# Kernel tuning notes

Hardware: AMD Instinct MI355X
Metric: run time of the kernel (lower is better)

## Reference

```python
import jax, jax.numpy as jnp
import numpy as np

IMG_W, IMG_H = 704, 256
BN_EPS, LN_EPS = 1e-5, 1e-5


def _l2norm(x, axis):
    n = jnp.linalg.norm(x, axis=axis, keepdims=True)
    return x / jnp.maximum(n, 1e-12)


def _layernorm(x, g, b):
    m = jnp.mean(x, axis=-1, keepdims=True)
    v = jnp.var(x, axis=-1, keepdims=True)
    return (x - m) / jnp.sqrt(v + LN_EPS) * g + b


def _bilinear(ref, uv):
    # ref: (B, d, H, W); uv: (B, P, 2) pixel coords (x, y)
    B, d, H, W = ref.shape
    x, y = uv[..., 0], uv[..., 1]
    x0 = jnp.floor(x); y0 = jnp.floor(y)
    wx = x - x0; wy = y - y0
    valid = (x >= 0) & (x <= W - 1) & (y >= 0) & (y <= H - 1)
    x0i = jnp.clip(x0.astype(jnp.int32), 0, W - 1)
    x1i = jnp.clip(x0i + 1, 0, W - 1)
    y0i = jnp.clip(y0.astype(jnp.int32), 0, H - 1)
    y1i = jnp.clip(y0i + 1, 0, H - 1)
    ref_t = ref.reshape(B, d, H * W).transpose(0, 2, 1)  # (B, HW, d)
    g = lambda yy, xx: jnp.take_along_axis(ref_t, (yy * W + xx)[..., None], axis=1)
    val = (g(y0i, x0i) * ((1 - wx) * (1 - wy))[..., None]
           + g(y0i, x1i) * (wx * (1 - wy))[..., None]
           + g(y1i, x0i) * ((1 - wx) * wy)[..., None]
           + g(y1i, x1i) * (wx * wy)[..., None])  # (B, P, d)
    return val, valid.astype(ref.dtype)


def setup_inputs() -> dict:
    key = jax.random.key(0)
    ks = jax.random.split(key, 12)
    b, n, fd, dim, h, w = 2, 6, 128, 128, 64, 176
    feature = jax.random.normal(ks[0], (b, n, fd, h, w), jnp.float32)
    # intrinsics ~ [[500,0,352],[0,500,128],[0,0,1]]
    K = jnp.array([[500.0, 0.0, IMG_W / 2], [0.0, 500.0, IMG_H / 2], [0.0, 0.0, 1.0]], jnp.float32)
    I_src = jnp.broadcast_to(K, (b, n, 3, 3)).copy()
    I_tar_inv = jnp.broadcast_to(jnp.linalg.inv(K), (b, 3, 3)).copy()
    # extrinsics near identity: small rotation + small translation
    a = 0.02 * jax.random.normal(ks[1], (b, n, 3), jnp.float32)
    zeros = jnp.zeros((b, n), jnp.float32)
    skew = jnp.stack([
        jnp.stack([zeros, -a[..., 2], a[..., 1]], -1),
        jnp.stack([a[..., 2], zeros, -a[..., 0]], -1),
        jnp.stack([-a[..., 1], a[..., 0], zeros], -1)], -2)
    R = jnp.eye(3, dtype=jnp.float32) + skew
    T = 0.1 * jax.random.normal(ks[2], (b, n, 3, 1), jnp.float32)
    E = jnp.broadcast_to(jnp.eye(4, dtype=jnp.float32), (b, n, 4, 4)).copy()
    E = E.at[..., :3, :3].set(R).at[..., :3, 3:4].set(T)
    dis = 1.5 * jnp.ones((b, 1, 1, 1), jnp.float32)
    norm = jnp.array([0.0, 0.0, 1.0], jnp.float32)[None, None] + 0.01 * jax.random.normal(ks[3], (b, 1, 3), jnp.float32)
    s = 1.0 / np.sqrt(fd)
    return {
        'feature': feature, 'I_src': I_src, 'I_tar_inv': I_tar_inv, 'E': E, 'dis': dis, 'norm': norm,
        'conv_w': s * jax.random.normal(ks[4], (dim, fd), jnp.float32),
        'bn_gamma': jnp.ones((fd,), jnp.float32), 'bn_beta': jnp.zeros((fd,), jnp.float32),
        'bn_mean': 0.1 * jax.random.normal(ks[5], (fd,), jnp.float32),
        'bn_var': jax.random.uniform(ks[6], (fd,), jnp.float32, 0.5, 1.5),
        'ln1_g': jnp.ones((dim,), jnp.float32), 'ln1_b': jnp.zeros((dim,), jnp.float32),
        'ln2_g': jnp.ones((dim,), jnp.float32), 'ln2_b': jnp.zeros((dim,), jnp.float32),
        'mlp_w1': s * jax.random.normal(ks[7], (dim, 2 * dim), jnp.float32),
        'mlp_b1': jnp.zeros((2 * dim,), jnp.float32),
        'mlp_w2': (1.0 / np.sqrt(2 * fd)) * jax.random.normal(ks[8], (2 * dim, dim), jnp.float32),
        'mlp_b2': jnp.zeros((dim,), jnp.float32),
    }


def reference(feature, I_src, I_tar_inv, E, dis, norm, conv_w, bn_gamma, bn_beta, bn_mean, bn_var,
              ln1_g, ln1_b, ln2_g, ln2_b, mlp_w1, mlp_b1, mlp_w2, mlp_b2):
    b, n, fd, h, w = feature.shape
    dim = conv_w.shape[0]
    P = h * w
    # ---- pixel grid in [0,1], homogeneous ----
    xs = jnp.linspace(0.0, 1.0, w, dtype=feature.dtype)
    ys = jnp.linspace(0.0, 1.0, h, dtype=feature.dtype)
    X, Y = jnp.meshgrid(xs, ys)  # (h, w), x varies along width
    pix = jnp.stack([X, Y, jnp.ones_like(X)], 0).reshape(3, P)  # (3, P)
    img_wh1 = jnp.array([[IMG_W], [IMG_H], [1.0]], feature.dtype)  # (3,1)
    pix = pix * img_wh1
    # ---- homography H = I_src (R - T n^T / dis) I_tar_inv ----
    R = E[..., :3, :3]
    T = E[..., :3, 3:4]
    Hm = I_src @ (R - (T @ norm[:, None, :, :]) / dis) @ I_tar_inv[:, None, :, :]  # (b,n,3,3)
    homo = jnp.einsum('bnij,jp->bnip', Hm, pix)  # (b,n,3,P)
    homo = homo[:, :, :2] / homo[:, :, 2:]
    homo = homo / img_wh1[:2]  # back to 0..1
    uv = homo.transpose(0, 1, 3, 2).reshape(b * n, P, 2) * jnp.array([w, h], feature.dtype)
    # ---- feature_linear: BN(eval) -> ReLU -> 1x1 conv ----
    xf = (feature - bn_mean[:, None, None]) / jnp.sqrt(bn_var + BN_EPS)[:, None, None]
    xf = xf * bn_gamma[:, None, None] + bn_beta[:, None, None]
    xf = jax.nn.relu(xf)
    val = jnp.einsum('oc,bnchw->bnohw', conv_w, xf)  # (b,n,dim,h,w)
    query = val[:, 0]  # (b,dim,h,w)
    # ---- homography-guided bilinear sampling ----
    v, mask = _bilinear(val.reshape(b * n, dim, h, w), uv)  # (bn,P,dim), (bn,P)
    key_n = _l2norm(v, axis=2).reshape(b, n, P, dim)
    q = _l2norm(query.reshape(b, dim, P), axis=1)
    dot = jnp.einsum('bdp,bnpd->bnp', q, key_n)
    dot = dot * mask.reshape(b, n, P)
    att = jax.nn.softmax(dot, axis=1)
    z = jnp.einsum('bnp,bnpd->bpd', att, v.reshape(b, n, P, dim))
    z = z.transpose(0, 2, 1).reshape(b, dim, h, w)
    z = query + z
    # ---- MLP block ----
    z = z.reshape(b, dim, P).transpose(0, 2, 1)  # (b,P,dim)
    z = _layernorm(z, ln1_g, ln1_b)
    hdn = jax.nn.gelu(z @ mlp_w1 + mlp_b1, approximate=False)
    z = z + (hdn @ mlp_w2 + mlp_b2)
    z = _layernorm(z, ln2_g, ln2_b)
    return z.transpose(0, 2, 1).reshape(b, dim, h, w)
```

## Files before the change

### kernel.cpp

```cpp
#include <hip/hip_runtime.h>
#include <hip/hip_bf16.h>
#include <cstdint>
#include <cstddef>

#define B_   2
#define N_   6
#define FD_  128
#define DIM_ 128
#define H_   64
#define W_   176
#define P_   (H_*W_)
#define IMGW 704.0
#define IMGH 256.0
#define UVB  8

struct __align__(16) Samp { float wx, wy; int o00, o01; int o10, o11; int valid, pad; };

typedef __attribute__((ext_vector_type(8))) short short8;
typedef __attribute__((ext_vector_type(4))) float f32x4;

__device__ __forceinline__ float wave_sum(float v) {
#pragma unroll
  for (int off = 32; off > 0; off >>= 1) v += __shfl_xor(v, off, 64);
  return v;
}

__device__ __forceinline__ unsigned short f2bf(float f) {
  union { __hip_bfloat16 h; unsigned short u; } c;
  c.h = __float2bfloat16(f);
  return c.u;
}
__device__ __forceinline__ float bf2f(unsigned short s) {
  return __uint_as_float(((unsigned int)s) << 16);
}
__device__ __forceinline__ float bfx(uint2 u, int j) {
  unsigned int w = (j < 2) ? u.x : u.y;
  return bf2f((unsigned short)((j & 1) ? (w >> 16) : (w & 0xffffu)));
}

__global__ __launch_bounds__(256) void prep_kernel(const float* __restrict__ I_src, const float* __restrict__ I_tar_inv,
                           const float* __restrict__ E, const float* __restrict__ dis,
                           const float* __restrict__ nrm,
                           const float* __restrict__ bn_g, const float* __restrict__ bn_b,
                           const float* __restrict__ bn_m, const float* __restrict__ bn_v,
                           const float* __restrict__ w1, const float* __restrict__ w2,
                           const float* __restrict__ conv_w,
                           Samp* __restrict__ samp, float* __restrict__ bns, float* __restrict__ bnb,
                           short* __restrict__ w1b, short* __restrict__ w2b, short* __restrict__ cwb) {
  int blk = blockIdx.x;
  if (blk >= B_ * N_ * UVB) {
    int tid = (blk - B_ * N_ * UVB) * 256 + threadIdx.x;
    int f = tid >> 6, l = tid & 63;
    if (f < 64) {
      int nt = f >> 2, ks = f & 3;
      int n = nt * 16 + (l & 15);
      int kb = ks * 32 + (l >> 4) * 8;
#pragma unroll
      for (int j = 0; j < 8; ++j)
        w1b[((size_t)f * 64 + l) * 8 + j] = (short)f2bf(w1[(size_t)(kb + j) * 256 + n]);
    } else if (f < 128) {
      int g = f - 64;
      int nt = g >> 3, ks = g & 7;
      int n = nt * 16 + (l & 15);
      int kb = ks * 32 + (l >> 4) * 8;
#pragma unroll
      for (int j = 0; j < 8; ++j)
        w2b[((size_t)g * 64 + l) * 8 + j] = (short)f2bf(w2[(size_t)(kb + j) * 128 + n]);
    } else {
      int g2 = f - 128;
      int ot = g2 >> 2, ks = g2 & 3;
      int o  = ot * 16 + (l & 15);
      int cb = ks * 32 + (l >> 4) * 8;
#pragma unroll
      for (int j = 0; j < 8; ++j)
        cwb[((size_t)g2 * 64 + l) * 8 + j] = (short)f2bf(conv_w[(size_t)o * FD_ + cb + j]);
    }
    return;
  }
  int bn = blk / UVB;
  int part = blk % UVB;
  int bb = bn / N_;
  if (blk == 0 && threadIdx.x < FD_) {
    int t = threadIdx.x;
    float inv = 1.0f / sqrtf(bn_v[t] + 1e-5f);
    float sc = bn_g[t] * inv;
    bns[t] = sc;
    bnb[t] = bn_b[t] - bn_m[t] * sc;
  }
  const float* Ep = E + bn * 16;
  double R[9], T[3];
#pragma unroll
  for (int i = 0; i < 3; ++i) {
#pragma unroll
    for (int j = 0; j < 3; ++j) R[i*3+j] = (double)Ep[i*4+j];
    T[i] = (double)Ep[i*4+3];
  }
  double dd = (double)dis[bb];
  double M[9];
#pragma unroll
  for (int i = 0; i < 3; ++i)
#pragma unroll
    for (int j = 0; j < 3; ++j)
      M[i*3+j] = R[i*3+j] - T[i] * (double)nrm[bb*3+j] / dd;
  const float* Is = I_src + bn * 9;
  double A[9];
#pragma unroll
  for (int i = 0; i < 3; ++i)
#pragma unroll
    for (int j = 0; j < 3; ++j)
      A[i*3+j] = (double)Is[i*3+0]*M[0+j] + (double)Is[i*3+1]*M[3+j] + (double)Is[i*3+2]*M[6+j];
  const float* It = I_tar_inv + bb * 9;
  double Hm[9];
#pragma unroll
  for (int i = 0; i < 3; ++i)
#pragma unroll
    for (int j = 0; j < 3; ++j)
      Hm[i*3+j] = A[i*3+0]*(double)It[0+j] + A[i*3+1]*(double)It[3+j] + A[i*3+2]*(double)It[6+j];

  const double dx = 1.0 / (double)(W_ - 1);
  const double dy = 1.0 / (double)(H_ - 1);
  for (int p = part * 256 + threadIdx.x; p < P_; p += 256 * UVB) {
    int ii = p / W_;
    int jj = p - ii * W_;
    double xs = (jj == W_ - 1) ? 1.0 : (double)jj * dx;
    double ys = (ii == H_ - 1) ? 1.0 : (double)ii * dy;
    double px = xs * IMGW;
    double py = ys * IMGH;
    double hx = Hm[0]*px + Hm[1]*py + Hm[2];
    double hy = Hm[3]*px + Hm[4]*py + Hm[5];
    double hz = Hm[6]*px + Hm[7]*py + Hm[8];
    double u = ((hx / hz) / IMGW) * (double)W_;
    double v = ((hy / hz) / IMGH) * (double)H_;
    double x0 = floor(u), y0 = floor(v);
    bool valid = (u >= 0.0) && (u <= (double)(W_ - 1)) && (v >= 0.0) && (v <= (double)(H_ - 1));
    int x0i = min(max((int)x0, 0), W_ - 1);
    int x1i = min(x0i + 1, W_ - 1);
    int y0i = min(max((int)y0, 0), H_ - 1);
    int y1i = min(y0i + 1, H_ - 1);
    Samp s;
    s.wx = (float)(u - x0);
    s.wy = (float)(v - y0);
    s.o00 = (y0i * W_ + x0i) * DIM_;
    s.o01 = (y0i * W_ + x1i) * DIM_;
    s.o10 = (y1i * W_ + x0i) * DIM_;
    s.o11 = (y1i * W_ + x1i) * DIM_;
    s.valid = valid ? 1 : 0;
    s.pad = 0;
    samp[(size_t)bn * P_ + p] = s;
  }
}

__global__ __launch_bounds__(256) void conv_kernel(const float* __restrict__ feature,
    const short* __restrict__ cwb, const float* __restrict__ bns_g, const float* __restrict__ bnb_g,
    unsigned short* __restrict__ val_t) {
  __shared__ float bns_s[FD_], bnb_s[FD_];
  int t = threadIdx.x;
  if (t < FD_) { bns_s[t] = bns_g[t]; bnb_s[t] = bnb_g[t]; }
  __syncthreads();

  int bn = blockIdx.y;
  int p0 = blockIdx.x * 64;
  int lane = t & 63, wv = t >> 6;
  int m = lane & 15, quad = lane >> 4;
  int pw = wv * 16;

  const float* fb = feature + (size_t)bn * FD_ * P_ + p0 + pw + m;

  float xv[4][8];
#pragma unroll
  for (int ks = 0; ks < 4; ++ks)
#pragma unroll
    for (int j = 0; j < 8; ++j) {
      int c = ks * 32 + quad * 8 + j;
      xv[ks][j] = fb[(size_t)c * P_];
    }

  short8 Ah[4], Al[4];
#pragma unroll
  for (int ks = 0; ks < 4; ++ks)
#pragma unroll
    for (int j = 0; j < 8; ++j) {
      int c = ks * 32 + quad * 8 + j;
      float v = fmaxf(xv[ks][j] * bns_s[c] + bnb_s[c], 0.f);
      unsigned short h = f2bf(v);
      Ah[ks][j] = (short)h;
      Al[ks][j] = (short)f2bf(v - bf2f(h));
    }

  f32x4 acc[8];
#pragma unroll
  for (int ot = 0; ot < 8; ++ot) {
    f32x4 a = {0.f, 0.f, 0.f, 0.f};
#pragma unroll
    for (int ks = 0; ks < 4; ++ks) {
      short8 Bv = *(const short8*)(cwb + ((size_t)(ot * 4 + ks) * 64 + lane) * 8);
      a = __builtin_amdgcn_mfma_f32_16x16x32_bf16(Ah[ks], Bv, a, 0, 0, 0);
      a = __builtin_amdgcn_mfma_f32_16x16x32_bf16(Al[ks], Bv, a, 0, 0, 0);
    }
    acc[ot] = a;
  }

  unsigned short* vb = val_t + ((size_t)bn * P_ + p0 + pw + quad * 4) * DIM_ + m;
#pragma unroll
  for (int ot = 0; ot < 8; ++ot)
#pragma unroll
    for (int r = 0; r < 4; ++r)
      vb[(size_t)r * DIM_ + ot * 16] = f2bf(acc[ot][r]);
}

__global__ __launch_bounds__(256) void attn_kernel(const unsigned short* __restrict__ val_t,
    const Samp* __restrict__ samp,
    const float* __restrict__ ln1g, const float* __restrict__ ln1b,
    float* __restrict__ zln) {
  int lane = threadIdx.x & 63;
  int wv = threadIdx.x >> 6;
  int half = lane >> 5;
  int sl = lane & 31;
  int bid = blockIdx.x;
  int newbid = (bid & 7) * (gridDim.x >> 3) + (bid >> 3);
  int pt = newbid * 8 + wv * 2 + half;
  int bb = pt / P_;
  int p = pt - bb * P_;
  int d0 = sl << 2;

  uint2 uq = *(const uint2*)(val_t + ((size_t)(bb * N_) * P_ + p) * DIM_ + d0);
  float qv[4] = { bfx(uq, 0), bfx(uq, 1), bfx(uq, 2), bfx(uq, 3) };
  float qss = qv[0]*qv[0] + qv[1]*qv[1] + qv[2]*qv[2] + qv[3]*qv[3];
#pragma unroll
  for (int off = 1; off <= 16; off <<= 1) qss += __shfl_xor(qss, off, 64);
  float qinv = 1.0f / fmaxf(sqrtf(qss), 1e-12f);

  float dots[N_], vs[N_][4];
#pragma unroll
  for (int n = 0; n < N_; ++n) {
    Samp s = samp[(size_t)(bb * N_ + n) * P_ + p];
    const unsigned short* base = val_t + (size_t)(bb * N_ + n) * P_ * DIM_ + d0;
    uint2 u00 = *(const uint2*)(base + s.o00);
    uint2 u01 = *(const uint2*)(base + s.o01);
    uint2 u10 = *(const uint2*)(base + s.o10);
    uint2 u11 = *(const uint2*)(base + s.o11);
    float wx = s.wx, wy = s.wy;
    float w00 = (1.0f - wx) * (1.0f - wy), w01 = wx * (1.0f - wy);
    float w10 = (1.0f - wx) * wy,          w11 = wx * wy;
    float ss = 0.f, du = 0.f;
#pragma unroll
    for (int j = 0; j < 4; ++j) {
      float v = bfx(u00, j) * w00 + bfx(u01, j) * w01 + bfx(u10, j) * w10 + bfx(u11, j) * w11;
      vs[n][j] = v;
      ss += v * v;
      du += qv[j] * v;
    }
#pragma unroll
    for (int off = 1; off <= 16; off <<= 1) {
      ss += __shfl_xor(ss, off, 64);
      du += __shfl_xor(du, off, 64);
    }
    float kinv = 1.0f / fmaxf(sqrtf(ss), 1e-12f);
    dots[n] = s.valid ? (du * kinv * qinv) : 0.0f;
  }
  float mx = dots[0];
#pragma unroll
  for (int n = 1; n < N_; ++n) mx = fmaxf(mx, dots[n]);
  float es[N_], den = 0.f;
#pragma unroll
  for (int n = 0; n < N_; ++n) { es[n] = expf(dots[n] - mx); den += es[n]; }
  float dinv = 1.0f / den;
  float z[4] = { qv[0], qv[1], qv[2], qv[3] };
#pragma unroll
  for (int n = 0; n < N_; ++n) {
    float a = es[n] * dinv;
#pragma unroll
    for (int j = 0; j < 4; ++j) z[j] += a * vs[n][j];
  }
  float sz = z[0] + z[1] + z[2] + z[3];
  float q2 = z[0]*z[0] + z[1]*z[1] + z[2]*z[2] + z[3]*z[3];
#pragma unroll
  for (int off = 1; off <= 16; off <<= 1) {
    sz += __shfl_xor(sz, off, 64);
    q2 += __shfl_xor(q2, off, 64);
  }
  float mean = sz * (1.0f / DIM_);
  float var = fmaxf(q2 * (1.0f / DIM_) - mean * mean, 0.f);
  float rstd = rsqrtf(var + 1e-5f);
  float4 g4 = *(const float4*)(ln1g + d0);
  float4 b4 = *(const float4*)(ln1b + d0);
  float4 o4;
  o4.x = (z[0] - mean) * rstd * g4.x + b4.x;
  o4.y = (z[1] - mean) * rstd * g4.y + b4.y;
  o4.z = (z[2] - mean) * rstd * g4.z + b4.z;
  o4.w = (z[3] - mean) * rstd * g4.w + b4.w;
  *(float4*)(zln + (size_t)pt * DIM_ + d0) = o4;
}

__global__ __launch_bounds__(64) void mlp_kernel(const float* __restrict__ zln,
    const short* __restrict__ w1b, const short* __restrict__ w2b,
    const float* __restrict__ b1, const float* __restrict__ b2,
    const float* __restrict__ ln2g, const float* __restrict__ ln2b,
    float* __restrict__ out) {
  __shared__ __align__(16) char smem[16896];
  short* hh = (short*)smem;
  short* hl = (short*)(smem + 8448);
  float* zo = (float*)smem;

  int l = threadIdx.x;
  int m = l & 15, quad = l >> 4;
  int row0 = blockIdx.x * 16;

  const float* zr0 = zln + (size_t)(row0 + m) * DIM_;
  short8 A1h[4], A1l[4];
#pragma unroll
  for (int ks = 0; ks < 4; ++ks) {
    float4 xa = *(const float4*)(zr0 + ks * 32 + quad * 8);
    float4 xb = *(const float4*)(zr0 + ks * 32 + quad * 8 + 4);
    float v[8] = {xa.x, xa.y, xa.z, xa.w, xb.x, xb.y, xb.z, xb.w};
#pragma unroll
    for (int j = 0; j < 8; ++j) {
      unsigned short h = f2bf(v[j]);
      A1h[ks][j] = (short)h;
      A1l[ks][j] = (short)f2bf(v[j] - bf2f(h));
    }
  }

  float res[8][4];
#pragma unroll
  for (int dt = 0; dt < 8; ++dt)
#pragma unroll
    for (int r = 0; r < 4; ++r)
      res[dt][r] = zln[(size_t)(row0 + quad * 4 + r) * DIM_ + dt * 16 + m];

  float b1v[16];
#pragma unroll
  for (int nt = 0; nt < 16; ++nt) b1v[nt] = b1[nt * 16 + m];
  float b2v[8], g2v[8], be2v[8];
#pragma unroll
  for (int dt = 0; dt < 8; ++dt) {
    int d = dt * 16 + m;
    b2v[dt] = b2[d]; g2v[dt] = ln2g[d]; be2v[dt] = ln2b[d];
  }

#pragma unroll
  for (int nt = 0; nt < 16; ++nt) {
    f32x4 a = {0.f, 0.f, 0.f, 0.f};
#pragma unroll
    for (int ks = 0; ks < 4; ++ks) {
      short8 Bv = *(const short8*)(w1b + ((size_t)(nt * 4 + ks) * 64 + l) * 8);
      a = __builtin_amdgcn_mfma_f32_16x16x32_bf16(A1h[ks], Bv, a, 0, 0, 0);
      a = __builtin_amdgcn_mfma_f32_16x16x32_bf16(A1l[ks], Bv, a, 0, 0, 0);
    }
#pragma unroll
    for (int r = 0; r < 4; ++r) {
      float hv = a[r] + b1v[nt];
      float g = 0.5f * hv * (1.0f + erff(hv * 0.70710678118654752f));
      unsigned short gh = f2bf(g);
      int addr = (quad * 4 + r) * 264 + nt * 16 + m;
      hh[addr] = (short)gh;
      hl[addr] = (short)f2bf(g - bf2f(gh));
    }
  }
  __syncthreads();

  f32x4 acc2[8];
#pragma unroll
  for (int dt = 0; dt < 8; ++dt) acc2[dt] = (f32x4){0.f, 0.f, 0.f, 0.f};
#pragma unroll
  for (int ks2 = 0; ks2 < 8; ++ks2) {
    short8 A2h = *(const short8*)&hh[m * 264 + ks2 * 32 + quad * 8];
    short8 A2l = *(const short8*)&hl[m * 264 + ks2 * 32 + quad * 8];
#pragma unroll
    for (int dt = 0; dt < 8; ++dt) {
      short8 Bv = *(const short8*)(w2b + ((size_t)(dt * 8 + ks2) * 64 + l) * 8);
      acc2[dt] = __builtin_amdgcn_mfma_f32_16x16x32_bf16(A2h, Bv, acc2[dt], 0, 0, 0);
      acc2[dt] = __builtin_amdgcn_mfma_f32_16x16x32_bf16(A2l, Bv, acc2[dt], 0, 0, 0);
    }
  }

  float z2[8][4];
#pragma unroll
  for (int dt = 0; dt < 8; ++dt)
#pragma unroll
    for (int r = 0; r < 4; ++r)
      z2[dt][r] = acc2[dt][r] + b2v[dt] + res[dt][r];

  float mean[4], rstd[4];
#pragma unroll
  for (int r = 0; r < 4; ++r) {
    float s = 0.f, q2 = 0.f;
#pragma unroll
    for (int dt = 0; dt < 8; ++dt) { float z = z2[dt][r]; s += z; q2 += z * z; }
#pragma unroll
    for (int off = 1; off <= 8; off <<= 1) {
      s  += __shfl_xor(s,  off, 64);
      q2 += __shfl_xor(q2, off, 64);
    }
    mean[r] = s * (1.0f / 128.0f);
    float var = fmaxf(q2 * (1.0f / 128.0f) - mean[r] * mean[r], 0.f);
    rstd[r] = rsqrtf(var + 1e-5f);
  }
  __syncthreads();

#pragma unroll
  for (int dt = 0; dt < 8; ++dt)
#pragma unroll
    for (int r = 0; r < 4; ++r) {
      float v = (z2[dt][r] - mean[r]) * rstd[r] * g2v[dt] + be2v[dt];
      zo[(dt * 16 + m) * 20 + quad * 4 + r] = v;
    }
  __syncthreads();

  int bb2 = row0 / P_;
  int p0 = row0 - bb2 * P_;
  float* ob = out + (size_t)bb2 * DIM_ * P_ + p0;
#pragma unroll
  for (int pass = 0; pass < 8; ++pass) {
    int idx = pass * 64 + l;
    int d = idx >> 2, fq = idx & 3;
    float4 v4 = *(float4*)&zo[d * 20 + fq * 4];
    *(float4*)(ob + (size_t)d * P_ + fq * 4) = v4;
  }
}

extern "C" void kernel_launch(void* const* d_in, const int* in_sizes, int n_in,
                              void* d_out, int out_size, void* d_ws, size_t ws_size,
                              hipStream_t stream) {
  const float* feature = (const float*)d_in[0];
  const float* I_src   = (const float*)d_in[1];
  const float* I_tar   = (const float*)d_in[2];
  const float* E       = (const float*)d_in[3];
  const float* dis     = (const float*)d_in[4];
  const float* nrm     = (const float*)d_in[5];
  const float* conv_w  = (const float*)d_in[6];
  const float* bn_g    = (const float*)d_in[7];
  const float* bn_b    = (const float*)d_in[8];
  const float* bn_m    = (const float*)d_in[9];
  const float* bn_v    = (const float*)d_in[10];
  const float* ln1g    = (const float*)d_in[11];
  const float* ln1b    = (const float*)d_in[12];
  const float* ln2g    = (const float*)d_in[13];
  const float* ln2b    = (const float*)d_in[14];
  const float* w1      = (const float*)d_in[15];
  const float* b1      = (const float*)d_in[16];
  const float* w2      = (const float*)d_in[17];
  const float* b2      = (const float*)d_in[18];
  float* out = (float*)d_out;

  float* wsf = (float*)d_ws;
  float* bns = wsf;
  float* bnb = wsf + 128;
  unsigned short* val_t = (unsigned short*)(wsf + 256);
  float* zln = (float*)(val_t + (size_t)B_ * N_ * P_ * DIM_);
  Samp*  samp = (Samp*)(zln + (size_t)B_ * P_ * DIM_);
  short* w1b = (short*)(samp + (size_t)B_ * N_ * P_);
  short* w2b = w1b + 32768;
  short* cwb = w2b + 32768;

  hipLaunchKernelGGL(prep_kernel, dim3(B_ * N_ * UVB + 40), dim3(256), 0, stream,
                     I_src, I_tar, E, dis, nrm, bn_g, bn_b, bn_m, bn_v, w1, w2, conv_w,
                     samp, bns, bnb, w1b, w2b, cwb);
  hipLaunchKernelGGL(conv_kernel, dim3(P_ / 64, B_ * N_), dim3(256), 0, stream,
                     feature, cwb, bns, bnb, val_t);
  hipLaunchKernelGGL(attn_kernel, dim3(B_ * P_ / 8), dim3(256), 0, stream,
                     val_t, samp, ln1g, ln1b, zln);
  hipLaunchKernelGGL(mlp_kernel, dim3(B_ * P_ / 16), dim3(64), 0, stream,
                     zln, w1b, w2b, b1, b2, ln2g, ln2b, out);
}
```

Before: 211.2 us.

## Split MLP kernel work across four waves per 16-row block

The MLP kernel now launches 256 threads per block instead of 64. Each of the four waves computes a quarter of the hidden-layer N-tiles and a quarter of the output D-tiles, and the LayerNorm row statistics are reduced across waves through a small shared-memory buffer. The goal is to cut per-wave register pressure and serial MFMA chain length and to raise parallelism per block. The cost is an extra barrier, and every wave redundantly loads the A fragments and splits them into hi/lo parts.

```diff
diff --git a/kernel.cpp b/kernel.cpp
--- a/kernel.cpp
+++ b/kernel.cpp
@@ -292,17 +292,19 @@
   *(float4*)(zln + (size_t)pt * DIM_ + d0) = o4;
 }
 
-__global__ __launch_bounds__(64) void mlp_kernel(const float* __restrict__ zln,
+__global__ __launch_bounds__(256) void mlp_kernel(const float* __restrict__ zln,
     const short* __restrict__ w1b, const short* __restrict__ w2b,
     const float* __restrict__ b1, const float* __restrict__ b2,
     const float* __restrict__ ln2g, const float* __restrict__ ln2b,
     float* __restrict__ out) {
-  __shared__ __align__(16) char smem[16896];
+  __shared__ __align__(16) char smem[17408];
   short* hh = (short*)smem;
   short* hl = (short*)(smem + 8448);
+  float* pbuf = (float*)(smem + 16896);
   float* zo = (float*)smem;
 
-  int l = threadIdx.x;
+  int t = threadIdx.x;
+  int l = t & 63, ng = t >> 6;
   int m = l & 15, quad = l >> 4;
   int row0 = blockIdx.x * 16;
 
@@ -321,25 +323,23 @@
     }
   }
 
-  float res[8][4];
-#pragma unroll
-  for (int dt = 0; dt < 8; ++dt)
+  float b1v[4];
+#pragma unroll
+  for (int i = 0; i < 4; ++i) b1v[i] = b1[(ng * 4 + i) * 16 + m];
+  float res[2][4], b2v[2], g2v[2], be2v[2];
+#pragma unroll
+  for (int e = 0; e < 2; ++e) {
+    int dt = ng * 2 + e;
+    int d = dt * 16 + m;
+    b2v[e] = b2[d]; g2v[e] = ln2g[d]; be2v[e] = ln2b[d];
 #pragma unroll
     for (int r = 0; r < 4; ++r)
-      res[dt][r] = zln[(size_t)(row0 + quad * 4 + r) * DIM_ + dt * 16 + m];
-
-  float b1v[16];
-#pragma unroll
-  for (int nt = 0; nt < 16; ++nt) b1v[nt] = b1[nt * 16 + m];
-  float b2v[8], g2v[8], be2v[8];
-#pragma unroll
-  for (int dt = 0; dt < 8; ++dt) {
-    int d = dt * 16 + m;
-    b2v[dt] = b2[d]; g2v[dt] = ln2g[d]; be2v[dt] = ln2b[d];
-  }
-
-#pragma unroll
-  for (int nt = 0; nt < 16; ++nt) {
+      res[e][r] = zln[(size_t)(row0 + quad * 4 + r) * DIM_ + dt * 16 + m];
+  }
+
+#pragma unroll
+  for (int i = 0; i < 4; ++i) {
+    int nt = ng * 4 + i;
     f32x4 a = {0.f, 0.f, 0.f, 0.f};
 #pragma unroll
     for (int ks = 0; ks < 4; ++ks) {
@@ -349,7 +349,7 @@
     }
 #pragma unroll
     for (int r = 0; r < 4; ++r) {
-      float hv = a[r] + b1v[nt];
+      float hv = a[r] + b1v[i];
       float g = 0.5f * hv * (1.0f + erff(hv * 0.70710678118654752f));
       unsigned short gh = f2bf(g);
       int addr = (quad * 4 + r) * 264 + nt * 16 + m;
@@ -359,60 +359,78 @@
   }
   __syncthreads();
 
-  f32x4 acc2[8];
-#pragma unroll
-  for (int dt = 0; dt < 8; ++dt) acc2[dt] = (f32x4){0.f, 0.f, 0.f, 0.f};
+  f32x4 acc2[2];
+  acc2[0] = (f32x4){0.f, 0.f, 0.f, 0.f};
+  acc2[1] = (f32x4){0.f, 0.f, 0.f, 0.f};
 #pragma unroll
   for (int ks2 = 0; ks2 < 8; ++ks2) {
     short8 A2h = *(const short8*)&hh[m * 264 + ks2 * 32 + quad * 8];
     short8 A2l = *(const short8*)&hl[m * 264 + ks2 * 32 + quad * 8];
 #pragma unroll
-    for (int dt = 0; dt < 8; ++dt) {
-      short8 Bv = *(const short8*)(w2b + ((size_t)(dt * 8 + ks2) * 64 + l) * 8);
-      acc2[dt] = __builtin_amdgcn_mfma_f32_16x16x32_bf16(A2h, Bv, acc2[dt], 0, 0, 0);
-      acc2[dt] = __builtin_amdgcn_mfma_f32_16x16x32_bf16(A2l, Bv, acc2[dt], 0, 0, 0);
-    }
-  }
-
-  float z2[8][4];
-#pragma unroll
-  for (int dt = 0; dt < 8; ++dt)
+    for (int e = 0; e < 2; ++e) {
+      int g = (ng * 2 + e) * 8 + ks2;
+      short8 Bv = *(const short8*)(w2b + ((size_t)g * 64 + l) * 8);
+      acc2[e] = __builtin_amdgcn_mfma_f32_16x16x32_bf16(A2h, Bv, acc2[e], 0, 0, 0);
+      acc2[e] = __builtin_amdgcn_mfma_f32_16x16x32_bf16(A2l, Bv, acc2[e], 0, 0, 0);
+    }
+  }
+
+  float z2[2][4];
+#pragma unroll
+  for (int e = 0; e < 2; ++e)
 #pragma unroll
     for (int r = 0; r < 4; ++r)
-      z2[dt][r] = acc2[dt][r] + b2v[dt] + res[dt][r];
-
-  float mean[4], rstd[4];
+      z2[e][r] = acc2[e][r] + b2v[e] + res[e][r];
+
+  float ps[4], pq2[4];
 #pragma unroll
   for (int r = 0; r < 4; ++r) {
-    float s = 0.f, q2 = 0.f;
-#pragma unroll
-    for (int dt = 0; dt < 8; ++dt) { float z = z2[dt][r]; s += z; q2 += z * z; }
+    float s = z2[0][r] + z2[1][r];
+    float q2 = z2[0][r]*z2[0][r] + z2[1][r]*z2[1][r];
 #pragma unroll
     for (int off = 1; off <= 8; off <<= 1) {
       s  += __shfl_xor(s,  off, 64);
       q2 += __shfl_xor(q2, off, 64);
     }
+    ps[r] = s; pq2[r] = q2;
+  }
+  if (m == 0) {
+#pragma unroll
+    for (int r = 0; r < 4; ++r) {
+      pbuf[ng * 16 + quad * 4 + r]      = ps[r];
+      pbuf[64 + ng * 16 + quad * 4 + r] = pq2[r];
+    }
+  }
+  __syncthreads();
+
+  float mean[4], rstd[4];
+#pragma unroll
+  for (int r = 0; r < 4; ++r) {
+    int px = quad * 4 + r;
+    float s = pbuf[px] + pbuf[16 + px] + pbuf[32 + px] + pbuf[48 + px];
+    float q = pbuf[64 + px] + pbuf[80 + px] + pbuf[96 + px] + pbuf[112 + px];
     mean[r] = s * (1.0f / 128.0f);
-    float var = fmaxf(q2 * (1.0f / 128.0f) - mean[r] * mean[r], 0.f);
+    float var = fmaxf(q * (1.0f / 128.0f) - mean[r] * mean[r], 0.f);
     rstd[r] = rsqrtf(var + 1e-5f);
   }
-  __syncthreads();
-
-#pragma unroll
-  for (int dt = 0; dt < 8; ++dt)
+
+#pragma unroll
+  for (int e = 0; e < 2; ++e) {
+    int dt = ng * 2 + e;
 #pragma unroll
     for (int r = 0; r < 4; ++r) {
-      float v = (z2[dt][r] - mean[r]) * rstd[r] * g2v[dt] + be2v[dt];
+      float v = (z2[e][r] - mean[r]) * rstd[r] * g2v[e] + be2v[e];
       zo[(dt * 16 + m) * 20 + quad * 4 + r] = v;
     }
+  }
   __syncthreads();
 
   int bb2 = row0 / P_;
   int p0 = row0 - bb2 * P_;
   float* ob = out + (size_t)bb2 * DIM_ * P_ + p0;
 #pragma unroll
-  for (int pass = 0; pass < 8; ++pass) {
-    int idx = pass * 64 + l;
+  for (int pass = 0; pass < 2; ++pass) {
+    int idx = pass * 256 + t;
     int d = idx >> 2, fq = idx & 3;
     float4 v4 = *(float4*)&zo[d * 20 + fq * 4];
     *(float4*)(ob + (size_t)d * P_ + fq * 4) = v4;
@@ -460,6 +478,6 @@
                      feature, cwb, bns, bnb, val_t);
   hipLaunchKernelGGL(attn_kernel, dim3(B_ * P_ / 8), dim3(256), 0, stream,
                      val_t, samp, ln1g, ln1b, zln);
-  hipLaunchKernelGGL(mlp_kernel, dim3(B_ * P_ / 16), dim3(64), 0, stream,
+  hipLaunchKernelGGL(mlp_kernel, dim3(B_ * P_ / 16), dim3(256), 0, stream,
                      zln, w1b, w2b, b1, b2, ln2g, ln2b, out);
 }
```

After: 194.4 us. 7.9% less time.

## Fuse attention and MLP kernels, splitting MLP tiles across eight waves

Applied to the files above, without the earlier changes.

Merges attn_kernel and mlp_kernel into one 512-thread kernel. Each block computes 16 attended, LayerNorm'd pixels into shared memory, then splits the MLP's hidden and output column tiles across its 8 waves. The second LayerNorm is reduced across waves through a small shared buffer. This removes the fp32 zln round trip through global memory and one kernel launch, at the cost of extra block barriers and higher shared memory per block, which may reduce occupancy.

```diff
diff --git a/kernel.cpp b/kernel.cpp
--- a/kernel.cpp
+++ b/kernel.cpp
@@ -18,12 +18,6 @@
 
 typedef __attribute__((ext_vector_type(8))) short short8;
 typedef __attribute__((ext_vector_type(4))) float f32x4;
-
-__device__ __forceinline__ float wave_sum(float v) {
-#pragma unroll
-  for (int off = 32; off > 0; off >>= 1) v += __shfl_xor(v, off, 64);
-  return v;
-}
 
 __device__ __forceinline__ unsigned short f2bf(float f) {
   union { __hip_bfloat16 h; unsigned short u; } c;
@@ -208,17 +202,29 @@
       vb[(size_t)r * DIM_ + ot * 16] = f2bf(acc[ot][r]);
 }
 
-__global__ __launch_bounds__(256) void attn_kernel(const unsigned short* __restrict__ val_t,
+__global__ __launch_bounds__(512) void attn_mlp_kernel(const unsigned short* __restrict__ val_t,
     const Samp* __restrict__ samp,
     const float* __restrict__ ln1g, const float* __restrict__ ln1b,
-    float* __restrict__ zln) {
-  int lane = threadIdx.x & 63;
-  int wv = threadIdx.x >> 6;
-  int half = lane >> 5;
-  int sl = lane & 31;
+    const short* __restrict__ w1b, const short* __restrict__ w2b,
+    const float* __restrict__ b1, const float* __restrict__ b2,
+    const float* __restrict__ ln2g, const float* __restrict__ ln2b,
+    float* __restrict__ out) {
+  __shared__ __align__(16) char smem[26368];
+  float* zl   = (float*)smem;
+  short* hh   = (short*)(smem + 8448);
+  short* hl   = (short*)(smem + 16896);
+  float* pbuf = (float*)(smem + 25344);
+  float* zo   = (float*)smem;
+
+  int t = threadIdx.x;
+  int l = t & 63, wv = t >> 6;
+  int half = l >> 5, sl = l & 31;
+  int m = l & 15, quad = (l >> 4) & 3;
   int bid = blockIdx.x;
   int newbid = (bid & 7) * (gridDim.x >> 3) + (bid >> 3);
-  int pt = newbid * 8 + wv * 2 + half;
+  int row0 = newbid * 16;
+
+  int pt = row0 + wv * 2 + half;
   int bb = pt / P_;
   int p = pt - bb * P_;
   int d0 = sl << 2;
@@ -279,67 +285,45 @@
     sz += __shfl_xor(sz, off, 64);
     q2 += __shfl_xor(q2, off, 64);
   }
-  float mean = sz * (1.0f / DIM_);
-  float var = fmaxf(q2 * (1.0f / DIM_) - mean * mean, 0.f);
-  float rstd = rsqrtf(var + 1e-5f);
+  float mean1 = sz * (1.0f / DIM_);
+  float var1 = fmaxf(q2 * (1.0f / DIM_) - mean1 * mean1, 0.f);
+  float rstd1 = rsqrtf(var1 + 1e-5f);
   float4 g4 = *(const float4*)(ln1g + d0);
   float4 b4 = *(const float4*)(ln1b + d0);
   float4 o4;
-  o4.x = (z[0] - mean) * rstd * g4.x + b4.x;
-  o4.y = (z[1] - mean) * rstd * g4.y + b4.y;
-  o4.z = (z[2] - mean) * rstd * g4.z + b4.z;
-  o4.w = (z[3] - mean) * rstd * g4.w + b4.w;
-  *(float4*)(zln + (size_t)pt * DIM_ + d0) = o4;
-}
-
-__global__ __launch_bounds__(64) void mlp_kernel(const float* __restrict__ zln,
-    const short* __restrict__ w1b, const short* __restrict__ w2b,
-    const float* __restrict__ b1, const float* __restrict__ b2,
-    const float* __restrict__ ln2g, const float* __restrict__ ln2b,
-    float* __restrict__ out) {
-  __shared__ __align__(16) char smem[16896];
-  short* hh = (short*)smem;
-  short* hl = (short*)(smem + 8448);
-  float* zo = (float*)smem;
-
-  int l = threadIdx.x;
-  int m = l & 15, quad = l >> 4;
-  int row0 = blockIdx.x * 16;
-
-  const float* zr0 = zln + (size_t)(row0 + m) * DIM_;
+  o4.x = (z[0] - mean1) * rstd1 * g4.x + b4.x;
+  o4.y = (z[1] - mean1) * rstd1 * g4.y + b4.y;
+  o4.z = (z[2] - mean1) * rstd1 * g4.z + b4.z;
+  o4.w = (z[3] - mean1) * rstd1 * g4.w + b4.w;
+  *(float4*)&zl[(wv * 2 + half) * 132 + d0] = o4;
+  __syncthreads();
+
+  float b1v[2];
+  b1v[0] = b1[(wv * 2 + 0) * 16 + m];
+  b1v[1] = b1[(wv * 2 + 1) * 16 + m];
+  int dd = wv * 16 + m;
+  float b2v = b2[dd], g2v = ln2g[dd], be2v = ln2b[dd];
+
   short8 A1h[4], A1l[4];
+  const float* zr0 = &zl[m * 132];
 #pragma unroll
   for (int ks = 0; ks < 4; ++ks) {
-    float4 xa = *(const float4*)(zr0 + ks * 32 + quad * 8);
-    float4 xb = *(const float4*)(zr0 + ks * 32 + quad * 8 + 4);
-    float v[8] = {xa.x, xa.y, xa.z, xa.w, xb.x, xb.y, xb.z, xb.w};
 #pragma unroll
     for (int j = 0; j < 8; ++j) {
-      unsigned short h = f2bf(v[j]);
+      float v = zr0[ks * 32 + quad * 8 + j];
+      unsigned short h = f2bf(v);
       A1h[ks][j] = (short)h;
-      A1l[ks][j] = (short)f2bf(v[j] - bf2f(h));
-    }
-  }
-
-  float res[8][4];
-#pragma unroll
-  for (int dt = 0; dt < 8; ++dt)
-#pragma unroll
-    for (int r = 0; r < 4; ++r)
-      res[dt][r] = zln[(size_t)(row0 + quad * 4 + r) * DIM_ + dt * 16 + m];
-
-  float b1v[16];
-#pragma unroll
-  for (int nt = 0; nt < 16; ++nt) b1v[nt] = b1[nt * 16 + m];
-  float b2v[8], g2v[8], be2v[8];
-#pragma unroll
-  for (int dt = 0; dt < 8; ++dt) {
-    int d = dt * 16 + m;
-    b2v[dt] = b2[d]; g2v[dt] = ln2g[d]; be2v[dt] = ln2b[d];
-  }
-
-#pragma unroll
-  for (int nt = 0; nt < 16; ++nt) {
+      A1l[ks][j] = (short)f2bf(v - bf2f(h));
+    }
+  }
+  float res[4];
+#pragma unroll
+  for (int r = 0; r < 4; ++r)
+    res[r] = zl[(quad * 4 + r) * 132 + dd];
+
+#pragma unroll
+  for (int i = 0; i < 2; ++i) {
+    int nt = wv * 2 + i;
     f32x4 a = {0.f, 0.f, 0.f, 0.f};
 #pragma unroll
     for (int ks = 0; ks < 4; ++ks) {
@@ -349,7 +333,7 @@
     }
 #pragma unroll
     for (int r = 0; r < 4; ++r) {
-      float hv = a[r] + b1v[nt];
+      float hv = a[r] + b1v[i];
       float g = 0.5f * hv * (1.0f + erff(hv * 0.70710678118654752f));
       unsigned short gh = f2bf(g);
       int addr = (quad * 4 + r) * 264 + nt * 16 + m;
@@ -359,61 +343,68 @@
   }
   __syncthreads();
 
-  f32x4 acc2[8];
-#pragma unroll
-  for (int dt = 0; dt < 8; ++dt) acc2[dt] = (f32x4){0.f, 0.f, 0.f, 0.f};
+  f32x4 acc2 = {0.f, 0.f, 0.f, 0.f};
 #pragma unroll
   for (int ks2 = 0; ks2 < 8; ++ks2) {
     short8 A2h = *(const short8*)&hh[m * 264 + ks2 * 32 + quad * 8];
     short8 A2l = *(const short8*)&hl[m * 264 + ks2 * 32 + quad * 8];
-#pragma unroll
-    for (int dt = 0; dt < 8; ++dt) {
-      short8 Bv = *(const short8*)(w2b + ((size_t)(dt * 8 + ks2) * 64 + l) * 8);
-      acc2[dt] = __builtin_amdgcn_mfma_f32_16x16x32_bf16(A2h, Bv, acc2[dt], 0, 0, 0);
-      acc2[dt] = __builtin_amdgcn_mfma_f32_16x16x32_bf16(A2l, Bv, acc2[dt], 0, 0, 0);
-    }
-  }
-
-  float z2[8][4];
-#pragma unroll
-  for (int dt = 0; dt < 8; ++dt)
-#pragma unroll
-    for (int r = 0; r < 4; ++r)
-      z2[dt][r] = acc2[dt][r] + b2v[dt] + res[dt][r];
+    short8 Bv = *(const short8*)(w2b + ((size_t)(wv * 8 + ks2) * 64 + l) * 8);
+    acc2 = __builtin_amdgcn_mfma_f32_16x16x32_bf16(A2h, Bv, acc2, 0, 0, 0);
+    acc2 = __builtin_amdgcn_mfma_f32_16x16x32_bf16(A2l, Bv, acc2, 0, 0, 0);
+  }
+
+  float z2[4];
+#pragma unroll
+  for (int r = 0; r < 4; ++r)
+    z2[r] = acc2[r] + b2v + res[r];
+
+  float ps[4], pq[4];
+#pragma unroll
+  for (int r = 0; r < 4; ++r) {
+    float s = z2[r], q = z2[r] * z2[r];
+#pragma unroll
+    for (int off = 1; off <= 8; off <<= 1) {
+      s += __shfl_xor(s, off, 64);
+      q += __shfl_xor(q, off, 64);
+    }
+    ps[r] = s; pq[r] = q;
+  }
+  if (m == 0) {
+#pragma unroll
+    for (int r = 0; r < 4; ++r) {
+      pbuf[wv * 16 + quad * 4 + r]       = ps[r];
+      pbuf[128 + wv * 16 + quad * 4 + r] = pq[r];
+    }
+  }
+  __syncthreads();
 
   float mean[4], rstd[4];
 #pragma unroll
   for (int r = 0; r < 4; ++r) {
-    float s = 0.f, q2 = 0.f;
-#pragma unroll
-    for (int dt = 0; dt < 8; ++dt) { float z = z2[dt][r]; s += z; q2 += z * z; }
-#pragma unroll
-    for (int off = 1; off <= 8; off <<= 1) {
-      s  += __shfl_xor(s,  off, 64);
-      q2 += __shfl_xor(q2, off, 64);
+    int px = quad * 4 + r;
+    float s = 0.f, q = 0.f;
+#pragma unroll
+    for (int w = 0; w < 8; ++w) {
+      s += pbuf[w * 16 + px];
+      q += pbuf[128 + w * 16 + px];
     }
     mean[r] = s * (1.0f / 128.0f);
-    float var = fmaxf(q2 * (1.0f / 128.0f) - mean[r] * mean[r], 0.f);
+    float var = fmaxf(q * (1.0f / 128.0f) - mean[r] * mean[r], 0.f);
     rstd[r] = rsqrtf(var + 1e-5f);
   }
-  __syncthreads();
-
-#pragma unroll
-  for (int dt = 0; dt < 8; ++dt)
-#pragma unroll
-    for (int r = 0; r < 4; ++r) {
-      float v = (z2[dt][r] - mean[r]) * rstd[r] * g2v[dt] + be2v[dt];
-      zo[(dt * 16 + m) * 20 + quad * 4 + r] = v;
-    }
+
+#pragma unroll
+  for (int r = 0; r < 4; ++r) {
+    float v = (z2[r] - mean[r]) * rstd[r] * g2v + be2v;
+    zo[(wv * 16 + m) * 20 + quad * 4 + r] = v;
+  }
   __syncthreads();
 
   int bb2 = row0 / P_;
   int p0 = row0 - bb2 * P_;
   float* ob = out + (size_t)bb2 * DIM_ * P_ + p0;
-#pragma unroll
-  for (int pass = 0; pass < 8; ++pass) {
-    int idx = pass * 64 + l;
-    int d = idx >> 2, fq = idx & 3;
+  {
+    int d = t >> 2, fq = t & 3;
     float4 v4 = *(float4*)&zo[d * 20 + fq * 4];
     *(float4*)(ob + (size_t)d * P_ + fq * 4) = v4;
   }
@@ -458,8 +449,6 @@
                      samp, bns, bnb, w1b, w2b, cwb);
   hipLaunchKernelGGL(conv_kernel, dim3(P_ / 64, B_ * N_), dim3(256), 0, stream,
                      feature, cwb, bns, bnb, val_t);
-  hipLaunchKernelGGL(attn_kernel, dim3(B_ * P_ / 8), dim3(256), 0, stream,
-                     val_t, samp, ln1g, ln1b, zln);
-  hipLaunchKernelGGL(mlp_kernel, dim3(B_ * P_ / 16), dim3(64), 0, stream,
-                     zln, w1b, w2b, b1, b2, ln2g, ln2b, out);
-}
+  hipLaunchKernelGGL(attn_mlp_kernel, dim3(B_ * P_ / 16), dim3(512), 0, stream,
+                     val_t, samp, ln1g, ln1b, w1b, w2b, b1, b2, ln2g, ln2b, out);
+}
```

After: 197.7 us. -6.4%, faster.
